# Performance work log

Hardware: AMD Instinct MI355X
Metric: run time of the kernel (lower is better)

## Reference

```python
import jax, jax.numpy as jnp
import numpy as np

B = 2048          # batch of tree nodes
C = 256           # num_classes (GRU input size)
HS = 512          # h_size
H2 = 2 * HS       # GRU hidden size
D = 8             # max_output_degree


def setup_inputs() -> dict:
    key = jax.random.key(0)
    ks = jax.random.split(key, 12)
    s_ih = 1.0 / np.sqrt(C)
    s_h = 1.0 / np.sqrt(H2)
    return {
        "parent_output_label": jax.random.uniform(ks[0], (B, C), dtype=jnp.float32),
        "parent_h": jax.random.normal(ks[1], (B, HS), dtype=jnp.float32),
        "encoding": jax.random.normal(ks[2], (B, HS), dtype=jnp.float32),
        # stacked GRUCell params over the D output-degree slots
        "W_ih": jax.random.uniform(ks[3], (D, 3 * H2, C), jnp.float32, -s_ih, s_ih),
        "W_hh": jax.random.uniform(ks[4], (D, 3 * H2, H2), jnp.float32, -s_h, s_h),
        "b_ih": jax.random.uniform(ks[5], (D, 3 * H2), jnp.float32, -s_h, s_h),
        "b_hh": jax.random.uniform(ks[6], (D, 3 * H2), jnp.float32, -s_h, s_h),
        # stacked linear_probs (2h -> 1) and linear_hiddens (2h -> h)
        "W_p": jax.random.uniform(ks[7], (D, H2), jnp.float32, -s_h, s_h),
        "b_p": jax.random.uniform(ks[8], (D,), jnp.float32, -s_h, s_h),
        "W_h": jax.random.uniform(ks[9], (D, HS, H2), jnp.float32, -s_h, s_h),
        "b_h": jax.random.uniform(ks[10], (D, HS), jnp.float32, -s_h, s_h),
    }


def _compute_state_probs(x, h0, W_ih, W_hh, b_ih, b_hh, W_p, b_p, W_h, b_h):
    # x: [B, C], h0: [B, H2]. All D GRUCells fused into batched einsums.
    gi = jnp.einsum("bc,dgc->bdg", x, W_ih) + b_ih[None]        # [B, D, 3*H2]
    gh = jnp.einsum("bh,dgh->bdg", h0, W_hh) + b_hh[None]       # [B, D, 3*H2]
    i_r, i_z, i_n = jnp.split(gi, 3, axis=-1)
    h_r, h_z, h_n = jnp.split(gh, 3, axis=-1)
    r = jax.nn.sigmoid(i_r + h_r)
    z = jax.nn.sigmoid(i_z + h_z)
    n = jnp.tanh(i_n + r * h_n)
    hn = (1.0 - z) * n + z * h0[:, None, :]                      # [B, D, H2]
    probs = jax.nn.sigmoid(jnp.einsum("bdh,dh->bd", hn, W_p) + b_p[None])  # [B, D]
    hc = jnp.einsum("bdh,dkh->bdk", hn, W_h) + b_h[None]         # [B, D, HS]
    h = jnp.tanh(jnp.sum(hc, axis=1))                            # activ over summed slot hiddens
    return h, probs


def reference(parent_output_label, parent_h, encoding,
              W_ih, W_hh, b_ih, b_hh, W_p, b_p, W_h, b_h):
    h0 = jnp.concatenate([parent_h, encoding], axis=1)           # [B, 2*h_size]
    return _compute_state_probs(parent_output_label, h0,
                                W_ih, W_hh, b_ih, b_hh, W_p, b_p, W_h, b_h)
```

## Files before the change

### kernel.cpp

```cpp
#include <hip/hip_runtime.h>


#define B_   2048
#define C_   256
#define HS_  512
#define H2_  1024
#define G3_  3072
#define D_   8
#define NG_  24576
#define KF_  1280

typedef __attribute__((ext_vector_type(8))) short bfrag;
typedef __attribute__((ext_vector_type(4))) float f32x4;
typedef __attribute__((ext_vector_type(4))) unsigned short u16x4;
typedef __attribute__((ext_vector_type(2))) unsigned int u32x2;

static __device__ __forceinline__ unsigned short f2bf(float f) {
  unsigned u = __float_as_uint(f);
  u = (u + 0x7FFFu + ((u >> 16) & 1u)) >> 16;
  return (unsigned short)u;
}
static __device__ __forceinline__ float bf2f(unsigned short s) {
  return __uint_as_float(((unsigned)s) << 16);
}
static __device__ __forceinline__ unsigned pack2bf(float a, float b) {
  return ((unsigned)f2bf(b) << 16) | (unsigned)f2bf(a);
}
static __device__ __forceinline__ float fast_sigmoid(float x) {
  return 1.f / (1.f + __expf(-x));
}
static __device__ __forceinline__ float fast_tanh(float x) {
  return 1.f - 2.f / (__expf(2.f * x) + 1.f);
}

__device__ __forceinline__ void load16(const void* g, void* l) {
  __builtin_amdgcn_global_load_lds((const __attribute__((address_space(1))) void*)g,
                                   (__attribute__((address_space(3))) void*)l,
                                   16, 0, 0);
}

__global__ __launch_bounds__(256) void pack_kernel(
    const float* __restrict__ x, const float* __restrict__ ph,
    const float* __restrict__ enc, const float* __restrict__ Wih,
    const float* __restrict__ Whh, const float* __restrict__ Wh,
    unsigned short* __restrict__ A, unsigned short* __restrict__ Bf,
    unsigned short* __restrict__ BWh)
{
  const long long total4 = 38273024LL / 4;
  const long long stride = (long long)gridDim.x * blockDim.x;
  for (long long i = (long long)blockIdx.x * blockDim.x + threadIdx.x;
       i < total4; i += stride) {
    long long o = i * 4;
    const float* src;
    unsigned short* dst;
    if (o < 2621440) {
      unsigned rel = (unsigned)o;
      unsigned b = rel / 1280u, c = rel % 1280u;
      if (c < 256) src = x + (size_t)b * 256 + c;
      else if (c < 768) src = ph + (size_t)b * 512 + (c - 256);
      else src = enc + (size_t)b * 512 + (c - 768);
      dst = A + rel;
    } else if (o < 34078720) {
      unsigned rel = (unsigned)(o - 2621440);
      unsigned grow = rel / 1280u, c = rel % 1280u;
      unsigned d = grow / 3072u, rr = grow - d * 3072u;
      unsigned hbb = rr / 192u, r3 = rr - hbb * 192u;
      unsigned g = r3 >> 6, hl = r3 & 63u;
      unsigned srow = d * 3072u + g * 1024u + hbb * 64u + hl;
      src = (c < 256) ? (Wih + (size_t)srow * 256 + c)
                      : (Whh + (size_t)srow * 1024 + (c - 256));
      dst = Bf + rel;
    } else {
      unsigned rel = (unsigned)(o - 34078720);
      unsigned kk = rel >> 13;
      unsigned r2 = rel & 8191;
      unsigned d = r2 >> 10, hh = r2 & 1023;
      src = Wh + ((size_t)d * 524288 + (size_t)kk * 1024 + hh);
      dst = BWh + rel;
    }
    float4 v = *(const float4*)src;
    ushort4 w;
    w.x = f2bf(v.x); w.y = f2bf(v.y); w.z = f2bf(v.z); w.w = f2bf(v.w);
    *(ushort4*)dst = w;
  }
}

__global__ __launch_bounds__(512, 2) void mega_gemm(
    const unsigned short* __restrict__ A, const unsigned short* __restrict__ Bf,
    const float* __restrict__ ph, const float* __restrict__ enc,
    const float* __restrict__ bih, const float* __restrict__ bhh,
    const float* __restrict__ Wp, unsigned short* __restrict__ hn,
    float* __restrict__ pacc)
{
  extern __shared__ char lds[];
  const int t = threadIdx.x;
  const int wave = t >> 6, lane = t & 63;
  const int wr = wave >> 2, wc = wave & 3;
  const int la = lane & 15, ls = lane >> 4;

  const int q8 = gridDim.x >> 3;
  const int orig = blockIdx.x;
  const int swz = (orig & 7) * q8 + (orig >> 3);
  const int brow = (swz & 7) << 8;
  const int cb = swz >> 3;
  const int bcol = cb * 192;
  const int d = cb >> 4, hb = cb & 15;
  const int nT = 20;

  const int srr = t >> 3;
  const int ssc = ((t & 7) ^ ((t >> 3) & 7)) << 3;

  auto stageA = [&](int kt, int buf, int hf) {
    const unsigned short* src = A + (size_t)(brow + hf * 128 + srr) * KF_ + kt * 64 + ssc;
    char* dst = lds + buf * 32768 + hf * 16384 + t * 16;
    load16(src, dst);
    load16(src + (size_t)64 * KF_, dst + 8192);
  };
  auto stageB = [&](int kt, int buf, int th) {
    const unsigned short* src = Bf + (size_t)(bcol + th * 64 + srr) * KF_ + kt * 64 + ssc;
    char* dst = lds + 65536 + buf * 24576 + th * 8192 + t * 16;
    load16(src, dst);
  };

  stageA(0, 0, 0); stageA(0, 0, 1);
  stageB(0, 0, 0); stageB(0, 0, 1); stageB(0, 0, 2);
  stageA(1, 1, 0); stageA(1, 1, 1);
  stageB(1, 1, 0); stageB(1, 1, 1); stageB(1, 1, 2);
  asm volatile("s_waitcnt vmcnt(7)" ::: "memory");
  __builtin_amdgcn_s_barrier();

  f32x4 acc[8][3];
#pragma unroll
  for (int m = 0; m < 8; ++m)
#pragma unroll
    for (int n = 0; n < 3; ++n) acc[m][n] = (f32x4){0.f, 0.f, 0.f, 0.f};

  const int c0 = (ls << 4) ^ ((la & 7) << 4);

#pragma unroll 1
  for (int kt = 0; kt < nT; ++kt) {
    const int buf = kt & 1;
    const int kt2 = (kt + 2 < nT) ? kt + 2 : nT - 1;
    const char* ab = lds + buf * 32768 + wr * 16384;
    const char* bb = lds + 65536 + buf * 24576;
    bfrag a0[4], a1a[4], a1b[4], a2[4], b0[3], b1[3];

#pragma unroll
    for (int m = 0; m < 4; ++m) {
      a1a[m] = *(const bfrag*)(ab + (m * 16 + la) * 128 + (c0 ^ 64));
      a0[m]  = *(const bfrag*)(ab + (m * 16 + la) * 128 + c0);
    }
#pragma unroll
    for (int n = 0; n < 3; ++n) {
      const int r = wc * 48 + n * 16 + la;
      b0[n] = *(const bfrag*)(bb + (r >> 6) * 8192 + (r & 63) * 128 + c0);
    }
    __builtin_amdgcn_s_barrier();
    __builtin_amdgcn_s_setprio(1);
#pragma unroll
    for (int m = 0; m < 4; ++m)
#pragma unroll
      for (int n = 0; n < 3; ++n)
        acc[m][n] = __builtin_amdgcn_mfma_f32_16x16x32_bf16(a0[m], b0[n], acc[m][n], 0, 0, 0);
    __builtin_amdgcn_s_setprio(0);
    __builtin_amdgcn_s_barrier();

#pragma unroll
    for (int m = 0; m < 4; ++m) {
      a1b[m] = *(const bfrag*)(ab + ((m + 4) * 16 + la) * 128 + (c0 ^ 64));
      a2[m]  = *(const bfrag*)(ab + ((m + 4) * 16 + la) * 128 + c0);
    }
    __builtin_amdgcn_s_barrier();
    __builtin_amdgcn_s_setprio(1);
#pragma unroll
    for (int m = 0; m < 4; ++m)
#pragma unroll
      for (int n = 0; n < 3; ++n)
        acc[m + 4][n] = __builtin_amdgcn_mfma_f32_16x16x32_bf16(a2[m], b0[n], acc[m + 4][n], 0, 0, 0);
    __builtin_amdgcn_s_setprio(0);
    asm volatile("s_waitcnt lgkmcnt(0)" ::: "memory");
    __builtin_amdgcn_s_barrier();

#pragma unroll
    for (int n = 0; n < 3; ++n) {
      const int r = wc * 48 + n * 16 + la;
      b1[n] = *(const bfrag*)(bb + (r >> 6) * 8192 + (r & 63) * 128 + (c0 ^ 64));
    }
    stageA(kt2, buf, 0);
    stageA(kt2, buf, 1);
    __builtin_amdgcn_s_barrier();
    __builtin_amdgcn_s_setprio(1);
#pragma unroll
    for (int m = 0; m < 4; ++m)
#pragma unroll
      for (int n = 0; n < 3; ++n)
        acc[m][n] = __builtin_amdgcn_mfma_f32_16x16x32_bf16(a1a[m], b1[n], acc[m][n], 0, 0, 0);
    __builtin_amdgcn_s_setprio(0);
    asm volatile("s_waitcnt lgkmcnt(0)" ::: "memory");
    __builtin_amdgcn_s_barrier();

    stageB(kt2, buf, 0);
    stageB(kt2, buf, 1);
    stageB(kt2, buf, 2);
    __builtin_amdgcn_s_barrier();
    __builtin_amdgcn_s_setprio(1);
#pragma unroll
    for (int m = 0; m < 4; ++m)
#pragma unroll
      for (int n = 0; n < 3; ++n)
        acc[m + 4][n] = __builtin_amdgcn_mfma_f32_16x16x32_bf16(a1b[m], b1[n], acc[m + 4][n], 0, 0, 0);
    __builtin_amdgcn_s_setprio(0);
    asm volatile("s_waitcnt vmcnt(7)" ::: "memory");
    __builtin_amdgcn_s_barrier();

    if (kt == 3) {
#pragma unroll
      for (int m = 0; m < 8; ++m)
#pragma unroll
        for (int n = 0; n < 3; ++n) {
          const int colb = wc * 48 + n * 16;
          if (colb >= 128) {
            const int hl = (colb & 63) + la;
            const int row = wr * 128 + m * 16 + ls * 4;
            u32x2 v;
            v[0] = pack2bf(acc[m][n][0], acc[m][n][1]);
            v[1] = pack2bf(acc[m][n][2], acc[m][n][3]);
            *(u32x2*)(lds + 114688 + hl * 520 + row * 2) = v;
            acc[m][n] = (f32x4){0.f, 0.f, 0.f, 0.f};
          }
        }
    }
  }

  __syncthreads();
#pragma unroll
  for (int m = 0; m < 8; ++m)
#pragma unroll
    for (int n = 0; n < 3; ++n) {
      const int col = wc * 48 + n * 16 + la;
      const int row = wr * 128 + m * 16 + ls * 4;
      u32x2 v;
      v[0] = pack2bf(acc[m][n][0], acc[m][n][1]);
      v[1] = pack2bf(acc[m][n][2], acc[m][n][3]);
      *(u32x2*)(lds + col * 520 + row * 2) = v;
    }
  __syncthreads();

  const unsigned short* lu = (const unsigned short*)lds;
  const int row = t >> 1, half = t & 1;
  const int grow = brow + row;
  const int hbase = hb * 64 + half * 32;
  const float* h0p = (hb < 8) ? (ph + (size_t)grow * 512 + hbase)
                              : (enc + (size_t)grow * 512 + hbase - 512);
  float partial = 0.f;
  u16x4 st;
#pragma unroll
  for (int jj = 0; jj < 8; ++jj) {
    const int hg = hbase + jj * 4;
    const f32x4 br_ = *(const f32x4*)(bih + d * 3072 + hg);
    const f32x4 hr_ = *(const f32x4*)(bhh + d * 3072 + hg);
    const f32x4 bz_ = *(const f32x4*)(bih + d * 3072 + 1024 + hg);
    const f32x4 hz_ = *(const f32x4*)(bhh + d * 3072 + 1024 + hg);
    const f32x4 bn_ = *(const f32x4*)(bih + d * 3072 + 2048 + hg);
    const f32x4 hn_ = *(const f32x4*)(bhh + d * 3072 + 2048 + hg);
    const f32x4 wp_ = *(const f32x4*)(Wp + d * 1024 + hg);
    const f32x4 h0_ = *(const f32x4*)(h0p + jj * 4);
#pragma unroll
    for (int i = 0; i < 4; ++i) {
      const int hl = half * 32 + jj * 4 + i;
      const float rp = bf2f(lu[hl * 260 + row]);
      const float zp = bf2f(lu[(64 + hl) * 260 + row]);
      const float sp = bf2f(lu[(128 + hl) * 260 + row]);
      const float ip = bf2f(lu[57344 + hl * 260 + row]);
      const float r = fast_sigmoid(rp + br_[i] + hr_[i]);
      const float z = fast_sigmoid(zp + bz_[i] + hz_[i]);
      const float nn = fast_tanh(ip + bn_[i] + r * (sp + hn_[i]));
      const float hv = (1.f - z) * nn + z * h0_[i];
      st[i] = f2bf(hv);
      partial += hv * wp_[i];
    }
    *(u16x4*)(hn + (size_t)grow * 8192 + d * 1024 + hg) = st;
  }
  partial += __shfl_xor(partial, 1);
  if (!half) atomicAdd(pacc + (size_t)grow * 8 + d, partial);
}

__global__ __launch_bounds__(256) void gemm_bt(
    const unsigned short* __restrict__ A, const unsigned short* __restrict__ Bt,
    float* __restrict__ out, int M, int N, int K, int kPerSlice)
{
  __shared__ unsigned short sA[128 * 32];
  __shared__ unsigned short sB[128 * 32];
  const int t = threadIdx.x;
  const int wave = t >> 6, lane = t & 63;
  const int wr = wave >> 1, wc = wave & 1;
  const int brow = blockIdx.y << 7;
  const int bcol = blockIdx.x << 7;
  const int kOff = blockIdx.z * kPerSlice;

  f32x4 acc[4][4];
#pragma unroll
  for (int m = 0; m < 4; m++)
#pragma unroll
    for (int n = 0; n < 4; n++) acc[m][n] = (f32x4){0.f, 0.f, 0.f, 0.f};

  const int srow = t >> 2;
  const int scol = (t & 3) << 3;
  const unsigned short* aSrc = A + (size_t)(brow + srow) * K + kOff + scol;
  const unsigned short* bSrc = Bt + (size_t)(bcol + srow) * K + kOff + scol;
  const size_t rowStep = (size_t)64 * K;
  unsigned short* dA0 = sA + wave * 512;
  unsigned short* dA1 = sA + 2048 + wave * 512;
  unsigned short* dB0 = sB + wave * 512;
  unsigned short* dB1 = sB + 2048 + wave * 512;

  const int la = lane & 15;
  const int lk = (lane >> 4) << 3;
  const int kSteps = kPerSlice >> 5;

  for (int ks = 0; ks < kSteps; ++ks) {
    load16(aSrc, dA0);
    load16(aSrc + rowStep, dA1);
    load16(bSrc, dB0);
    load16(bSrc + rowStep, dB1);
    aSrc += 32; bSrc += 32;
    __syncthreads();
    bfrag aF[4], bF[4];
#pragma unroll
    for (int m = 0; m < 4; m++)
      aF[m] = *(const bfrag*)&sA[(wr * 64 + m * 16 + la) * 32 + lk];
#pragma unroll
    for (int n = 0; n < 4; n++)
      bF[n] = *(const bfrag*)&sB[(wc * 64 + n * 16 + la) * 32 + lk];
#pragma unroll
    for (int m = 0; m < 4; m++)
#pragma unroll
      for (int n = 0; n < 4; n++)
        acc[m][n] = __builtin_amdgcn_mfma_f32_16x16x32_bf16(aF[m], bF[n], acc[m][n], 0, 0, 0);
    __syncthreads();
  }

  const int orow = brow + wr * 64 + (lane >> 4) * 4;
  const int ocol = bcol + wc * 64 + la;
  float* o = out + (size_t)blockIdx.z * ((size_t)M * N);
#pragma unroll
  for (int m = 0; m < 4; m++) {
    const int rb = orow + m * 16;
#pragma unroll
    for (int n = 0; n < 4; n++) {
      const int cb = ocol + n * 16;
#pragma unroll
      for (int r = 0; r < 4; r++)
        o[(size_t)(rb + r) * N + cb] = acc[m][n][r];
    }
  }
}

__global__ __launch_bounds__(256) void reduce_h_kernel(
    const float* __restrict__ part, const float* __restrict__ b_h,
    float* __restrict__ hout)
{
  const int idx = blockIdx.x * 256 + threadIdx.x;
  const int kk = idx & 511;
  float s = 0.f;
#pragma unroll
  for (int sl = 0; sl < 16; ++sl) s += part[(size_t)sl * 1048576 + idx];
  float bias = 0.f;
#pragma unroll
  for (int d = 0; d < 8; ++d) bias += b_h[d * 512 + kk];
  hout[idx] = fast_tanh(s + bias);
}

__global__ __launch_bounds__(256) void probs_final(
    const float* __restrict__ pacc, const float* __restrict__ b_p,
    float* __restrict__ pout)
{
  const int i = blockIdx.x * 256 + threadIdx.x;
  pout[i] = fast_sigmoid(pacc[i] + b_p[i & 7]);
}

extern "C" void kernel_launch(void* const* d_in, const int* in_sizes, int n_in,
                              void* d_out, int out_size, void* d_ws, size_t ws_size,
                              hipStream_t stream) {
  const float* x   = (const float*)d_in[0];
  const float* ph  = (const float*)d_in[1];
  const float* enc = (const float*)d_in[2];
  const float* Wih = (const float*)d_in[3];
  const float* Whh = (const float*)d_in[4];
  const float* bih = (const float*)d_in[5];
  const float* bhh = (const float*)d_in[6];
  const float* Wp  = (const float*)d_in[7];
  const float* bp  = (const float*)d_in[8];
  const float* Wh  = (const float*)d_in[9];
  const float* bh  = (const float*)d_in[10];
  float* out = (float*)d_out;
  char* ws = (char*)d_ws;

  unsigned short* A    = (unsigned short*)(ws + 0);
  unsigned short* Bf   = (unsigned short*)(ws + 5242880);
  unsigned short* BWh  = (unsigned short*)(ws + 68157440);
  unsigned short* hn   = (unsigned short*)(ws + 76546048);
  float*          part = (float*)(ws + 110100480);
  float*          pacc = (float*)(ws + 177209344);

  hipFuncSetAttribute((const void*)mega_gemm,
                      hipFuncAttributeMaxDynamicSharedMemorySize, 147968);

  hipMemsetAsync(pacc, 0, 2048 * 8 * sizeof(float), stream);

  pack_kernel<<<2048, 256, 0, stream>>>(x, ph, enc, Wih, Whh, Wh, A, Bf, BWh);

  mega_gemm<<<1024, 512, 147968, stream>>>(A, Bf, ph, enc, bih, bhh, Wp, hn, pacc);

  dim3 g3(HS_ / 128, B_ / 128, 16);
  gemm_bt<<<g3, 256, 0, stream>>>(hn, BWh, part, B_, HS_, 8192, 512);

  reduce_h_kernel<<<4096, 256, 0, stream>>>(part, bh, out);

  probs_final<<<64, 256, 0, stream>>>(pacc, bp, out + 1048576);
}
```

Measured before the change: 274.5 us.

## Load full k-tile fragments up front and collapse GEMM loop to two phases

Restructures the main MFMA loop: all A and B fragments for both k-halves are read from LDS at once, and the four compute phases become two, with fewer barriers. Global prefetch of tile kt+2 is issued in one batch after the first phase and skipped on the last iterations, with a full vmcnt(0) drain at the tail in place of redundant reloads of the final tile. This cuts barrier count and redundant staging, but raises register pressure (16 A fragments live) and gives less interleaving of LDS reads with MFMA.

```diff
diff --git a/kernel.cpp b/kernel.cpp
--- a/kernel.cpp
+++ b/kernel.cpp
@@ -140,77 +140,56 @@
 #pragma unroll 1
   for (int kt = 0; kt < nT; ++kt) {
     const int buf = kt & 1;
-    const int kt2 = (kt + 2 < nT) ? kt + 2 : nT - 1;
     const char* ab = lds + buf * 32768 + wr * 16384;
     const char* bb = lds + 65536 + buf * 24576;
-    bfrag a0[4], a1a[4], a1b[4], a2[4], b0[3], b1[3];
-
-#pragma unroll
-    for (int m = 0; m < 4; ++m) {
-      a1a[m] = *(const bfrag*)(ab + (m * 16 + la) * 128 + (c0 ^ 64));
-      a0[m]  = *(const bfrag*)(ab + (m * 16 + la) * 128 + c0);
-    }
+    bfrag a0[8], a1[8], b0[3], b1[3];
+
+#pragma unroll
+    for (int m = 0; m < 8; ++m)
+      a0[m] = *(const bfrag*)(ab + (m * 16 + la) * 128 + c0);
 #pragma unroll
     for (int n = 0; n < 3; ++n) {
       const int r = wc * 48 + n * 16 + la;
       b0[n] = *(const bfrag*)(bb + (r >> 6) * 8192 + (r & 63) * 128 + c0);
     }
+#pragma unroll
+    for (int m = 0; m < 8; ++m)
+      a1[m] = *(const bfrag*)(ab + (m * 16 + la) * 128 + (c0 ^ 64));
+#pragma unroll
+    for (int n = 0; n < 3; ++n) {
+      const int r = wc * 48 + n * 16 + la;
+      b1[n] = *(const bfrag*)(bb + (r >> 6) * 8192 + (r & 63) * 128 + (c0 ^ 64));
+    }
     __builtin_amdgcn_s_barrier();
     __builtin_amdgcn_s_setprio(1);
 #pragma unroll
-    for (int m = 0; m < 4; ++m)
+    for (int m = 0; m < 8; ++m)
 #pragma unroll
       for (int n = 0; n < 3; ++n)
         acc[m][n] = __builtin_amdgcn_mfma_f32_16x16x32_bf16(a0[m], b0[n], acc[m][n], 0, 0, 0);
     __builtin_amdgcn_s_setprio(0);
-    __builtin_amdgcn_s_barrier();
-
-#pragma unroll
-    for (int m = 0; m < 4; ++m) {
-      a1b[m] = *(const bfrag*)(ab + ((m + 4) * 16 + la) * 128 + (c0 ^ 64));
-      a2[m]  = *(const bfrag*)(ab + ((m + 4) * 16 + la) * 128 + c0);
-    }
-    __builtin_amdgcn_s_barrier();
-    __builtin_amdgcn_s_setprio(1);
-#pragma unroll
-    for (int m = 0; m < 4; ++m)
-#pragma unroll
-      for (int n = 0; n < 3; ++n)
-        acc[m + 4][n] = __builtin_amdgcn_mfma_f32_16x16x32_bf16(a2[m], b0[n], acc[m + 4][n], 0, 0, 0);
-    __builtin_amdgcn_s_setprio(0);
     asm volatile("s_waitcnt lgkmcnt(0)" ::: "memory");
     __builtin_amdgcn_s_barrier();
 
-#pragma unroll
-    for (int n = 0; n < 3; ++n) {
-      const int r = wc * 48 + n * 16 + la;
-      b1[n] = *(const bfrag*)(bb + (r >> 6) * 8192 + (r & 63) * 128 + (c0 ^ 64));
-    }
-    stageA(kt2, buf, 0);
-    stageA(kt2, buf, 1);
-    __builtin_amdgcn_s_barrier();
+    if (kt + 2 < nT) {
+      stageA(kt + 2, buf, 0);
+      stageA(kt + 2, buf, 1);
+      stageB(kt + 2, buf, 0);
+      stageB(kt + 2, buf, 1);
+      stageB(kt + 2, buf, 2);
+    }
     __builtin_amdgcn_s_setprio(1);
 #pragma unroll
-    for (int m = 0; m < 4; ++m)
+    for (int m = 0; m < 8; ++m)
 #pragma unroll
       for (int n = 0; n < 3; ++n)
-        acc[m][n] = __builtin_amdgcn_mfma_f32_16x16x32_bf16(a1a[m], b1[n], acc[m][n], 0, 0, 0);
+        acc[m][n] = __builtin_amdgcn_mfma_f32_16x16x32_bf16(a1[m], b1[n], acc[m][n], 0, 0, 0);
     __builtin_amdgcn_s_setprio(0);
-    asm volatile("s_waitcnt lgkmcnt(0)" ::: "memory");
-    __builtin_amdgcn_s_barrier();
-
-    stageB(kt2, buf, 0);
-    stageB(kt2, buf, 1);
-    stageB(kt2, buf, 2);
-    __builtin_amdgcn_s_barrier();
-    __builtin_amdgcn_s_setprio(1);
-#pragma unroll
-    for (int m = 0; m < 4; ++m)
-#pragma unroll
-      for (int n = 0; n < 3; ++n)
-        acc[m + 4][n] = __builtin_amdgcn_mfma_f32_16x16x32_bf16(a1b[m], b1[n], acc[m + 4][n], 0, 0, 0);
-    __builtin_amdgcn_s_setprio(0);
-    asm volatile("s_waitcnt vmcnt(7)" ::: "memory");
+    if (kt + 2 < nT) {
+      asm volatile("s_waitcnt vmcnt(7)" ::: "memory");
+    } else {
+      asm volatile("s_waitcnt vmcnt(0)" ::: "memory");
+    }
     __builtin_amdgcn_s_barrier();
 
     if (kt == 3) {
```

After: 275.4 us. Within noise of the previous version (+0.3%).
